# Kernel tuning notes

Hardware: AMD Instinct MI355X
Metric: run time of the kernel (lower is better)

## Reference

```python
import jax, jax.numpy as jnp
import numpy as np

N_CLASSES = 18

def setup_inputs() -> dict:
    key = jax.random.key(0)
    k1, k2 = jax.random.split(key)
    B = 2_000_000
    output = jax.random.normal(k1, (B, N_CLASSES), dtype=jnp.float32)
    labels_soft = jax.random.uniform(k2, (B, N_CLASSES), dtype=jnp.float32)
    return {"output": output, "labels_soft": labels_soft}

def reference(output, labels_soft):
    # Original: sum over classes of mean_b( CE(output, cls) * labels_soft[:, cls] )
    # = mean over batch of sum_c( -log_softmax(output)[b, c] * labels_soft[b, c] )
    logp = jax.nn.log_softmax(output, axis=-1)          # [B, C]
    per_row = -jnp.sum(logp * labels_soft, axis=-1)     # [B]
    return jnp.mean(per_row)
```

## Files before the change

kernel.cpp:

```cpp
#include <hip/hip_runtime.h>

#define NCLS 18

__global__ __launch_bounds__(256) void ce_soft_kernel(
    const float* __restrict__ logits,
    const float* __restrict__ labels,
    float* __restrict__ result,
    int B, float invB)
{
    int tid = blockIdx.x * blockDim.x + threadIdx.x;
    int stride = gridDim.x * blockDim.x;

    float acc = 0.0f;
    for (int row = tid; row < B; row += stride) {
        const float2* o2 = (const float2*)(logits + (size_t)row * NCLS);
        const float2* l2 = (const float2*)(labels + (size_t)row * NCLS);
        float x[NCLS], l[NCLS];
        #pragma unroll
        for (int k = 0; k < NCLS / 2; ++k) {
            float2 v = o2[k];
            x[2 * k] = v.x; x[2 * k + 1] = v.y;
        }
        #pragma unroll
        for (int k = 0; k < NCLS / 2; ++k) {
            float2 w = l2[k];
            l[2 * k] = w.x; l[2 * k + 1] = w.y;
        }

        float m = x[0];
        #pragma unroll
        for (int c = 1; c < NCLS; ++c) m = fmaxf(m, x[c]);

        float se = 0.0f, dot = 0.0f, sl = 0.0f;
        #pragma unroll
        for (int c = 0; c < NCLS; ++c) {
            se += __expf(x[c] - m);
            dot = fmaf(l[c], x[c], dot);
            sl += l[c];
        }
        float lse = m + __logf(se);
        acc = fmaf(sl, lse, acc - dot);
    }

    #pragma unroll
    for (int off = 32; off > 0; off >>= 1)
        acc += __shfl_down(acc, off, 64);

    __shared__ float wave_sums[4];
    int lane = threadIdx.x & 63;
    int wid  = threadIdx.x >> 6;
    if (lane == 0) wave_sums[wid] = acc;
    __syncthreads();
    if (threadIdx.x == 0) {
        float s = wave_sums[0] + wave_sums[1] + wave_sums[2] + wave_sums[3];
        atomicAdd(result, s * invB);
    }
}

extern "C" void kernel_launch(void* const* d_in, const int* in_sizes, int n_in,
                              void* d_out, int out_size, void* d_ws, size_t ws_size,
                              hipStream_t stream) {
    const float* logits = (const float*)d_in[0];
    const float* labels = (const float*)d_in[1];
    float* result = (float*)d_out;

    int B = in_sizes[0] / NCLS;

    hipMemsetAsync(d_out, 0, sizeof(float), stream);

    int block = 256;
    int grid  = 2048;
    ce_soft_kernel<<<grid, block, 0, stream>>>(logits, labels, result, B, 1.0f / (float)B);
}
```

Before: 292.6 us.

## Stage logit tiles into LDS via global_load_lds and stream labels coalesced

Each block now processes 256-row tiles: logits are copied straight into shared memory with the direct global-to-LDS load builtin, each thread computes its row's log-sum-exp from LDS, and labels are then read as fully coalesced float2 words combined with the staged logits and LSE values. This replaces the per-thread strided 72-byte row reads, which coalesce poorly, with contiguous wide accesses. It adds three barriers per tile with no overlap between loading and compute, and a scalar tail loop for leftover rows.

New measurement: 294.9 us. No clear change (+0.8%).

```diff
diff --git a/kernel.cpp b/kernel.cpp
--- a/kernel.cpp
+++ b/kernel.cpp
@@ -1,6 +1,12 @@
 #include <hip/hip_runtime.h>
 
-#define NCLS 18
+#define NCLS   18
+#define TROWS  256
+#define TWORDS (TROWS * NCLS)
+#define NCHUNK ((TWORDS * 4) / 1024)
+
+#define AS1 __attribute__((address_space(1)))
+#define AS3 __attribute__((address_space(3)))
 
 __global__ __launch_bounds__(256) void ce_soft_kernel(
     const float* __restrict__ logits,
@@ -8,29 +14,72 @@
     float* __restrict__ result,
     int B, float invB)
 {
-    int tid = blockIdx.x * blockDim.x + threadIdx.x;
-    int stride = gridDim.x * blockDim.x;
+    __shared__ float sX[TWORDS];
+    __shared__ float sLse[TROWS];
 
+    const int tid  = threadIdx.x;
+    const int lane = tid & 63;
+    const int wid  = tid >> 6;
+
+    const int nTiles = B / TROWS;
     float acc = 0.0f;
-    for (int row = tid; row < B; row += stride) {
+
+    for (int tile = blockIdx.x; tile < nTiles; tile += gridDim.x) {
+        const float* gx = logits + (size_t)tile * TWORDS;
+
+        for (int c = wid; c < NCHUNK; c += 4) {
+            __builtin_amdgcn_global_load_lds(
+                (const AS1 void*)(gx + c * 256 + lane * 4),
+                (AS3 void*)(sX + c * 256),
+                16, 0, 0);
+        }
+        __syncthreads();
+
+        {
+            const float2* r2 = (const float2*)(sX + tid * NCLS);
+            float x[NCLS];
+            #pragma unroll
+            for (int k = 0; k < NCLS / 2; ++k) {
+                float2 v = r2[k];
+                x[2 * k] = v.x; x[2 * k + 1] = v.y;
+            }
+            float m = x[0];
+            #pragma unroll
+            for (int c = 1; c < NCLS; ++c) m = fmaxf(m, x[c]);
+            float se = 0.0f;
+            #pragma unroll
+            for (int c = 0; c < NCLS; ++c) se += __expf(x[c] - m);
+            sLse[tid] = m + __logf(se);
+        }
+        __syncthreads();
+
+        const float2* gl2 = (const float2*)(labels + (size_t)tile * TWORDS);
+        const float2* sx2 = (const float2*)sX;
+        #pragma unroll
+        for (int it = 0; it < TWORDS / 512; ++it) {
+            int j = it * 256 + tid;
+            float2 lv = gl2[j];
+            float2 xv = sx2[j];
+            float lse = sLse[j / 9];
+            acc = fmaf(lv.x, lse - xv.x, acc);
+            acc = fmaf(lv.y, lse - xv.y, acc);
+        }
+        __syncthreads();
+    }
+
+    for (int row = nTiles * TROWS + blockIdx.x * blockDim.x + tid; row < B;
+         row += gridDim.x * blockDim.x) {
         const float2* o2 = (const float2*)(logits + (size_t)row * NCLS);
         const float2* l2 = (const float2*)(labels + (size_t)row * NCLS);
         float x[NCLS], l[NCLS];
         #pragma unroll
         for (int k = 0; k < NCLS / 2; ++k) {
-            float2 v = o2[k];
-            x[2 * k] = v.x; x[2 * k + 1] = v.y;
+            float2 v = o2[k]; x[2 * k] = v.x; x[2 * k + 1] = v.y;
+            float2 w = l2[k]; l[2 * k] = w.x; l[2 * k + 1] = w.y;
         }
-        #pragma unroll
-        for (int k = 0; k < NCLS / 2; ++k) {
-            float2 w = l2[k];
-            l[2 * k] = w.x; l[2 * k + 1] = w.y;
-        }
-
         float m = x[0];
         #pragma unroll
         for (int c = 1; c < NCLS; ++c) m = fmaxf(m, x[c]);
-
         float se = 0.0f, dot = 0.0f, sl = 0.0f;
         #pragma unroll
         for (int c = 0; c < NCLS; ++c) {
@@ -47,11 +96,9 @@
         acc += __shfl_down(acc, off, 64);
 
     __shared__ float wave_sums[4];
-    int lane = threadIdx.x & 63;
-    int wid  = threadIdx.x >> 6;
     if (lane == 0) wave_sums[wid] = acc;
     __syncthreads();
-    if (threadIdx.x == 0) {
+    if (tid == 0) {
         float s = wave_sums[0] + wave_sums[1] + wave_sums[2] + wave_sums[3];
         atomicAdd(result, s * invB);
     }
```
